# Optimization experiments

Hardware: AMD Instinct MI355X
Metric: run time of the kernel (lower is better)

Reference implementation:

```python
import jax, jax.numpy as jnp
import numpy as np

P, M, N, H, B, E, K = 50, 512, 1024, 256, 8, 400, 5
ALPHA_MAX, TAU_MAX, RHO_MAX, ETA_MAX = 0.01, 1.0, 1.0, 1.0
LEAK = 0.01  # F.leaky_relu default slope


def _lrelu(x):
    return jnp.where(x >= 0, x, LEAK * x)


def _layernorm(x, g, b, eps=1e-5):
    mu = jnp.mean(x, axis=-1, keepdims=True)
    var = jnp.mean((x - mu) ** 2, axis=-1, keepdims=True)
    return (x - mu) * jax.lax.rsqrt(var + eps) * g + b


def setup_inputs() -> dict:
    ks = iter(jax.random.split(jax.random.key(0), 16))

    def w(fin, fout):
        return jax.random.normal(next(ks), (fin, fout), jnp.float32) * np.float32(np.sqrt(2.0 / (fin + fout)))

    H4 = 4 * H
    inp = {
        'A': jax.random.normal(next(ks), (1, P, M, N), jnp.float32) * 0.05,
        'b': jax.random.normal(next(ks), (B, P, M, 1), jnp.float32),
        'W1': w(2 * N, H), 'b1': jnp.zeros(H), 'bn1_s': jnp.ones(H), 'bn1_t': jnp.zeros(H),
        'W2': w(H, 2 * H), 'b2': jnp.zeros(2 * H), 'bn2_s': jnp.ones(2 * H), 'bn2_t': jnp.zeros(2 * H),
        'W3': w(2 * H, H4), 'b3': jnp.zeros(H4), 'bn3_s': jnp.ones(H4), 'bn3_t': jnp.zeros(H4),
        'W4': w(H4, H4), 'b4': jnp.zeros(H4), 'bn4_s': jnp.ones(H4), 'bn4_t': jnp.zeros(H4),
        'W5': w(H4, H4), 'b5': jnp.zeros(H4), 'bn5_s': jnp.ones(H4), 'bn5_t': jnp.zeros(H4),
        'ln_g': jnp.ones(H4), 'ln_b': jnp.zeros(H4),
        'Wd1': w(P * H4, H4), 'bd1': jnp.zeros(H4), 'lnd1_g': jnp.ones(H4), 'lnd1_b': jnp.zeros(H4),
        'Wd2': w(H4, 2 * H), 'bd2': jnp.zeros(2 * H), 'lnd2_g': jnp.ones(2 * H), 'lnd2_b': jnp.zeros(2 * H),
        'Wd3': w(2 * H, H), 'bd3': jnp.zeros(H), 'lnd3_g': jnp.ones(H), 'lnd3_b': jnp.zeros(H),
        'Wfc': w(H, 4) * 0.1, 'bfc': jnp.zeros(4),
        'edge_index': jax.random.randint(next(ks), (2, E), 0, P),
    }
    return inp


def reference(A, b, W1, b1, bn1_s, bn1_t, W2, b2, bn2_s, bn2_t, W3, b3, bn3_s, bn3_t,
              W4, b4, bn4_s, bn4_t, W5, b5, bn5_s, bn5_t, ln_g, ln_b,
              Wd1, bd1, lnd1_g, lnd1_b, Wd2, bd2, lnd2_g, lnd2_b, Wd3, bd3, lnd3_g, lnd3_b,
              Wfc, bfc, edge_index):
    A0 = A[0]                                             # [P,M,N]
    AtA = jnp.einsum('pmi,pmj->pij', A0, A0)              # [P,N,N]  (compute_Atx(A))
    Atb = jnp.einsum('pmn,bpm->bpn', A0, b[..., 0])[..., None]  # [B,P,N,1]

    src, dst = edge_index[0], edge_index[1]
    ones_e = jnp.ones((E,), A.dtype)
    # sum_neighbors: out-degree of each node p, shape broadcastable to [B,P,1,1]
    sum_nb = jax.ops.segment_sum(ones_e, src, num_segments=P)[None, :, None, None]

    # GCNConv normalization with self loops: norm_ij = deg_i^-1/2 * deg_j^-1/2
    sl = jnp.arange(P)
    src_a = jnp.concatenate([src, sl])
    dst_a = jnp.concatenate([dst, sl])
    deg = jax.ops.segment_sum(jnp.ones((E + P,), A.dtype), dst_a, num_segments=P)
    dinv = jax.lax.rsqrt(deg)
    coef = (dinv[src_a] * dinv[dst_a])[:, None]           # [E+P,1]

    convs = [(W1, b1, bn1_s, bn1_t), (W2, b2, bn2_s, bn2_t), (W3, b3, bn3_s, bn3_t),
             (W4, b4, bn4_s, bn4_t), (W5, b5, bn5_s, bn5_t)]

    def gconv(x, W, bias):                                # x: [P,Cin]
        xw = x @ W
        return jax.ops.segment_sum(xw[src_a] * coef, dst_a, num_segments=P) + bias

    def encode_one(feat):                                 # feat: [P,2N]
        x = feat
        for (W, bias, s, t) in convs:
            # leaky_relu -> BatchNorm1d (eval: affine scale/shift) -> dropout (eval: id)
            x = _lrelu(gconv(x, W, bias)) * s + t
        return _layernorm(x, ln_g, ln_b).reshape(-1)      # [P*4H]

    enc = jax.vmap(encode_one)

    y = jnp.zeros((B, P, N, 1), A.dtype)
    U = jnp.zeros_like(y)
    delta = jnp.zeros_like(y)
    Ys = []
    for k in range(K):
        AtAy = jnp.einsum('pij,bpj->bpi', AtA, y[..., 0])[..., None]  # [B,P,N,1]
        feat = jnp.concatenate([AtAy, Atb], axis=2)[..., 0]           # [B,P,2N]
        code = enc(feat)                                              # [B,P*4H]
        h = _lrelu(_layernorm(code @ Wd1 + bd1, lnd1_g, lnd1_b))
        h = _lrelu(_layernorm(h @ Wd2 + bd2, lnd2_g, lnd2_b))
        h = _lrelu(_layernorm(h @ Wd3 + bd3, lnd3_g, lnd3_b))
        hyp = jnp.clip(jax.nn.sigmoid(h @ Wfc + bfc), 1e-4, 0.99).reshape(B, 4, 1, 1, 1)
        alpha = hyp[:, 0] * ALPHA_MAX
        tau = hyp[:, 1] * TAU_MAX
        rho = hyp[:, 2] * RHO_MAX
        eta = hyp[:, 3] * ETA_MAX
        g = AtAy - Atb + jnp.sign(y) * tau + U * sum_nb + delta * rho
        mg = max(30.0, 100.0 - k)
        g = jnp.clip(g, -mg, mg)
        mv = max(10.0, 200.0 - k * 3)
        y = jnp.clip(y - alpha * g, -mv, mv)
        # compute_delta: for each directed edge (s,d): delta[s]+= (y_s-y_d); delta[d]-= (y_s-y_d)
        diff = y[:, src] - y[:, dst]                                  # [B,E,N,1]
        delta = jnp.zeros_like(y).at[:, src].add(diff).at[:, dst].add(-diff)
        U = jnp.clip(U + delta * eta, -mv, mv)
        Ys.append(y)
    return jnp.stack(Ys)                                              # [K,B,P,N,1]
```

## Files before the change

### kernel.cpp

```cpp
#include <hip/hip_runtime.h>

#define PP 50
#define MM 512
#define NN 1024

constexpr size_t F_ATB   = 0;
constexpr size_t F_ATAY  = F_ATB   + 409600;
constexpr size_t F_Y     = F_ATAY  + 409600;
constexpr size_t F_U     = F_Y     + 409600;
constexpr size_t F_DELTA = F_U     + 409600;
constexpr size_t F_BT    = F_DELTA + 409600;
constexpr size_t F_AYT   = F_BT    + 204800;
constexpr size_t F_Z     = F_AYT   + 204800;
constexpr size_t F_X0    = F_Z     + 917504;
constexpr size_t F_X1    = F_X0    + 409600;
constexpr size_t F_CODET = F_X1    + 409600;
constexpr size_t F_PART  = F_CODET + 409600;
constexpr size_t F_DPART = F_PART  + 3670016;
constexpr size_t F_DPART2= F_DPART + 2097152;
constexpr size_t F_H1    = F_DPART2+ 32768;
constexpr size_t F_H2    = F_H1    + 8192;
constexpr size_t F_H3    = F_H2    + 4096;
constexpr size_t F_HYP   = F_H3    + 2048;
constexpr size_t F_GCCO  = F_HYP   + 64;
constexpr size_t F_SUMNB = F_GCCO  + 512;
constexpr size_t F_END   = F_SUMNB + 64;

__device__ __forceinline__ float lrelu(float v) { return v >= 0.f ? v : 0.01f * v; }

__device__ __forceinline__ void bred2(float& s1, float& s2, float* sm) {
  #pragma unroll
  for (int off = 32; off > 0; off >>= 1) {
    s1 += __shfl_down(s1, off);
    s2 += __shfl_down(s2, off);
  }
  int w = threadIdx.x >> 6, l = threadIdx.x & 63;
  if (l == 0) { sm[w] = s1; sm[4 + w] = s2; }
  __syncthreads();
  s1 = sm[0] + sm[1] + sm[2] + sm[3];
  s2 = sm[4] + sm[5] + sm[6] + sm[7];
}

__global__ __launch_bounds__(512) void ksetup(const int* __restrict__ ei, float* sumnb,
                                              float* gccoef, int* gcoff, int* gcsrc,
                                              int* nbroff, int* nbridx) {
  __shared__ int cin[PP];
  __shared__ int cou[PP];
  __shared__ float sdinv[PP];
  __shared__ int goff[PP + 1], noff[PP + 1];
  int t = threadIdx.x;
  const int* src = ei;
  const int* dst = ei + 400;
  if (t < PP) { cin[t] = 0; cou[t] = 0; }
  __syncthreads();
  if (t < 400) {
    atomicAdd(&cou[src[t]], 1);
    atomicAdd(&cin[dst[t]], 1);
  }
  __syncthreads();
  if (t < PP) {
    sdinv[t] = rsqrtf((float)(cin[t] + 1));
    sumnb[t] = (float)cou[t];
  }
  __syncthreads();
  if (t == 0) {
    goff[0] = 0; noff[0] = 0;
    for (int p = 0; p < PP; ++p) {
      goff[p + 1] = goff[p] + cin[p] + 1;
      noff[p + 1] = noff[p] + cin[p] + cou[p];
    }
  }
  __syncthreads();
  if (t <= PP) { gcoff[t] = goff[t]; nbroff[t] = noff[t]; }
  if (t < 400) {
    int d = dst[t], s = src[t];
    int slot = 0;
    for (int e = 0; e < t; ++e) slot += (dst[e] == d) ? 1 : 0;
    int pos = goff[d] + slot;
    gcsrc[pos] = s;
    gccoef[pos] = sdinv[s] * sdinv[d];
  }
  if (t < PP) {
    int pos = goff[t] + cin[t];
    gcsrc[pos] = t;
    gccoef[pos] = sdinv[t] * sdinv[t];
  }
  if (t < 400) {
    int s = src[t], d = dst[t];
    int so = 0, si = 0;
    for (int e = 0; e < t; ++e) {
      so += (src[e] == s) ? 1 : 0;
      si += (dst[e] == d) ? 1 : 0;
    }
    nbridx[noff[s] + so] = d;
    nbridx[noff[d] + cou[d] + si] = s;
  }
}

__global__ __launch_bounds__(256) void kbt(const float* __restrict__ b, float* __restrict__ bt) {
  int i = blockIdx.x * 256 + threadIdx.x;
  int bb = i / (PP * MM);
  int r = i - bb * (PP * MM);
  bt[r * 8 + bb] = b[i];
}

__global__ __launch_bounds__(256) void katz(const float* __restrict__ A, const float* __restrict__ q,
                                            float* __restrict__ outv) {
  __shared__ float red[4][64][8];
  int nb = blockIdx.x, p = blockIdx.y, t = threadIdx.x;
  int ln = t & 63, mg = t >> 6;
  int n = nb * 64 + ln;
  float acc[8] = {0, 0, 0, 0, 0, 0, 0, 0};
  const float* ap = A + ((size_t)p * MM + mg * 128) * NN + n;
  const float* qp = q + ((size_t)p * MM + mg * 128) * 8;
  for (int m0 = 0; m0 < 128; m0 += 8) {
    float av[8];
    #pragma unroll
    for (int u = 0; u < 8; ++u) av[u] = ap[(size_t)(m0 + u) * NN];
    #pragma unroll
    for (int u = 0; u < 8; ++u) {
      #pragma unroll
      for (int bb = 0; bb < 8; ++bb) acc[bb] += av[u] * qp[(m0 + u) * 8 + bb];
    }
  }
  #pragma unroll
  for (int bb = 0; bb < 8; ++bb) red[mg][ln][bb] = acc[bb];
  __syncthreads();
  if (mg == 0) {
    #pragma unroll
    for (int bb = 0; bb < 8; ++bb) {
      float v = red[0][ln][bb] + red[1][ln][bb] + red[2][ln][bb] + red[3][ln][bb];
      outv[((size_t)bb * PP + p) * NN + n] = v;
    }
  }
}

__global__ __launch_bounds__(256) void kay(const float* __restrict__ A, const float* __restrict__ y,
                                           float* __restrict__ ayt) {
  __shared__ __align__(16) float sy[8][NN];
  int p = blockIdx.x, mb = blockIdx.y, t = threadIdx.x;
  #pragma unroll
  for (int bb = 0; bb < 8; ++bb)
    for (int n = t; n < NN; n += 256) sy[bb][n] = y[(bb * PP + p) * NN + n];
  __syncthreads();
  int w = t >> 6, l = t & 63;
  int mbase = mb * 64 + w * 16;
  for (int i = 0; i < 8; ++i) {
    int m0 = mbase + 2 * i, m1 = m0 + 1;
    float acc0[8] = {0, 0, 0, 0, 0, 0, 0, 0};
    float acc1[8] = {0, 0, 0, 0, 0, 0, 0, 0};
    const float* a0p = A + ((size_t)p * MM + m0) * NN;
    const float* a1p = a0p + NN;
    #pragma unroll
    for (int jj = 0; jj < 4; ++jj) {
      int n0 = 4 * l + 256 * jj;
      float4 a0 = *(const float4*)(a0p + n0);
      float4 a1 = *(const float4*)(a1p + n0);
      #pragma unroll
      for (int bb = 0; bb < 8; ++bb) {
        float4 yv = *(const float4*)&sy[bb][n0];
        acc0[bb] += a0.x * yv.x + a0.y * yv.y + a0.z * yv.z + a0.w * yv.w;
        acc1[bb] += a1.x * yv.x + a1.y * yv.y + a1.z * yv.z + a1.w * yv.w;
      }
    }
    #pragma unroll
    for (int off = 32; off > 0; off >>= 1) {
      #pragma unroll
      for (int bb = 0; bb < 8; ++bb) {
        acc0[bb] += __shfl_down(acc0[bb], off);
        acc1[bb] += __shfl_down(acc1[bb], off);
      }
    }
    if (l == 0) {
      #pragma unroll
      for (int bb = 0; bb < 8; ++bb) {
        ayt[((size_t)p * MM + m0) * 8 + bb] = acc0[bb];
        ayt[((size_t)p * MM + m1) * 8 + bb] = acc1[bb];
      }
    }
  }
}

__global__ __launch_bounds__(256) void kgather1(const float* __restrict__ atay,
                                                const float* __restrict__ atb,
                                                float* __restrict__ z,
                                                const int* __restrict__ gcoff,
                                                const int* __restrict__ gcsrc,
                                                const float* __restrict__ gccoef, int first) {
  int r = blockIdx.x, cc = blockIdx.y, t = threadIdx.x;
  size_t zi = (size_t)r * 2048 + (size_t)cc * 256 + t;
  if (r >= 400) { z[zi] = 0.f; return; }
  int srcA = (cc < 4) ? 1 : 0;
  if (srcA && first) { z[zi] = 0.f; return; }
  int b = r / 50, p = r - b * 50;
  int c = (srcA ? cc * 256 : (cc - 4) * 256) + t;
  const float* src = srcA ? atay : atb;
  float acc = 0.f;
  int o0 = gcoff[p], o1 = gcoff[p + 1];
  for (int idx = o0; idx < o1; ++idx)
    acc += gccoef[idx] * src[((size_t)b * 50 + gcsrc[idx]) * 1024 + c];
  z[zi] = acc;
}

__global__ __launch_bounds__(256) void kgatherX(const float* __restrict__ x, float* __restrict__ z,
                                                int Cin, const int* __restrict__ gcoff,
                                                const int* __restrict__ gcsrc,
                                                const float* __restrict__ gccoef) {
  int r = blockIdx.x, cc = blockIdx.y, t = threadIdx.x;
  int c = cc * 256 + t;
  size_t zi = (size_t)r * Cin + c;
  if (r >= 400) { z[zi] = 0.f; return; }
  int b = r / 50, p = r - b * 50;
  float acc = 0.f;
  int o0 = gcoff[p], o1 = gcoff[p + 1];
  for (int idx = o0; idx < o1; ++idx)
    acc += gccoef[idx] * x[((size_t)b * 50 + gcsrc[idx]) * Cin + c];
  z[zi] = acc;
}

__global__ __launch_bounds__(256) void kgemm(const float* __restrict__ X, const float* __restrict__ W,
                                             float* __restrict__ part, int K, int C, int krange) {
  int cb = blockIdx.x, rb = blockIdx.y, s = blockIdx.z;
  int t = threadIdx.x;
  __shared__ __align__(16) float As[16][64];
  __shared__ __align__(16) float Bs[16][68];
  int rbase = rb * 64, cbase = cb * 64;
  int k0 = s * krange, kend = k0 + krange;
  float acc[4][4] = {};
  int tx = t & 15, ty = t >> 4;
  int lrow = t >> 2, lk = (t & 3) * 4;
  int brow = t >> 4, bc = (t & 15) * 4;
  for (int k = k0; k < kend; k += 16) {
    float4 av = *(const float4*)(X + (size_t)(rbase + lrow) * K + k + lk);
    As[lk + 0][lrow] = av.x;
    As[lk + 1][lrow] = av.y;
    As[lk + 2][lrow] = av.z;
    As[lk + 3][lrow] = av.w;
    *(float4*)&Bs[brow][bc] = *(const float4*)(W + (size_t)(k + brow) * C + cbase + bc);
    __syncthreads();
    #pragma unroll
    for (int kk = 0; kk < 16; ++kk) {
      float4 a = *(const float4*)&As[kk][ty * 4];
      float4 b = *(const float4*)&Bs[kk][tx * 4];
      float aa[4] = {a.x, a.y, a.z, a.w};
      float bb[4] = {b.x, b.y, b.z, b.w};
      #pragma unroll
      for (int i = 0; i < 4; ++i)
        #pragma unroll
        for (int j = 0; j < 4; ++j) acc[i][j] += aa[i] * bb[j];
    }
    __syncthreads();
  }
  #pragma unroll
  for (int i = 0; i < 4; ++i) {
    int r = rbase + ty * 4 + i;
    *(float4*)&part[((size_t)s * 448 + r) * C + cbase + tx * 4] =
        make_float4(acc[i][0], acc[i][1], acc[i][2], acc[i][3]);
  }
}

template <int NCH, bool LASTLN>
__global__ __launch_bounds__(256) void kredE(const float* __restrict__ part, int S,
                                             const float* __restrict__ bias,
                                             const float* __restrict__ bns,
                                             const float* __restrict__ bnt,
                                             float* __restrict__ xout,
                                             const float* __restrict__ lng,
                                             const float* __restrict__ lnb,
                                             float* __restrict__ codet) {
  __shared__ float smr[8];
  constexpr int C = NCH * 256;
  int r = blockIdx.x, t = threadIdx.x;
  float vals[NCH];
  #pragma unroll
  for (int ch = 0; ch < NCH; ++ch) {
    int c = ch * 256 + t;
    float acc = 0.f;
    const float* pp = part + (size_t)r * C + c;
    #pragma unroll 4
    for (int s = 0; s < S; ++s) acc += pp[(size_t)s * 448 * C];
    float v = lrelu(acc + bias[c]);
    vals[ch] = v * bns[c] + bnt[c];
  }
  if (!LASTLN) {
    #pragma unroll
    for (int ch = 0; ch < NCH; ++ch)
      xout[(size_t)r * C + ch * 256 + t] = vals[ch];
  } else {
    float s1 = 0.f, s2 = 0.f;
    #pragma unroll
    for (int ch = 0; ch < NCH; ++ch) { s1 += vals[ch]; s2 += vals[ch] * vals[ch]; }
    bred2(s1, s2, smr);
    float mu = s1 / (float)C;
    float var = s2 / (float)C - mu * mu;
    float rs = rsqrtf(var + 1e-5f);
    int b = r / 50, p = r - b * 50;
    #pragma unroll
    for (int ch = 0; ch < NCH; ++ch) {
      int c = ch * 256 + t;
      codet[((size_t)p * C + c) * 8 + b] = (vals[ch] - mu) * rs * lng[c] + lnb[c];
    }
  }
}

__global__ __launch_bounds__(256) void kwd1(const float* __restrict__ W,
                                            const float* __restrict__ in_t,
                                            float* __restrict__ dpart) {
  int t = threadIdx.x, s = blockIdx.x;
  int k0 = s * 200;
  float4 acc[8];
  #pragma unroll
  for (int b = 0; b < 8; ++b) acc[b] = make_float4(0.f, 0.f, 0.f, 0.f);
  const float* wp = W + (size_t)k0 * 1024 + 4 * t;
  const float* qp = in_t + (size_t)k0 * 8;
  for (int k = 0; k < 200; k += 4) {
    float4 wv[4], qa[4], qb[4];
    #pragma unroll
    for (int u = 0; u < 4; ++u) {
      wv[u] = *(const float4*)(wp + (size_t)(k + u) * 1024);
      qa[u] = *(const float4*)(qp + (k + u) * 8);
      qb[u] = *(const float4*)(qp + (k + u) * 8 + 4);
    }
    #pragma unroll
    for (int u = 0; u < 4; ++u) {
      float qs[8] = {qa[u].x, qa[u].y, qa[u].z, qa[u].w, qb[u].x, qb[u].y, qb[u].z, qb[u].w};
      #pragma unroll
      for (int b = 0; b < 8; ++b) {
        acc[b].x += wv[u].x * qs[b];
        acc[b].y += wv[u].y * qs[b];
        acc[b].z += wv[u].z * qs[b];
        acc[b].w += wv[u].w * qs[b];
      }
    }
  }
  #pragma unroll
  for (int b = 0; b < 8; ++b)
    *(float4*)&dpart[(size_t)(s * 8 + b) * 1024 + 4 * t] = acc[b];
}

__global__ __launch_bounds__(256) void kredA(const float* __restrict__ dpart,
                                             float* __restrict__ dpart2) {
  int cb = blockIdx.x, sg = blockIdx.y, b = blockIdx.z, t = threadIdx.x;
  int c = cb * 256 + t;
  float acc = 0.f;
  const float* pp = dpart + ((size_t)(sg * 64) * 8 + b) * 1024 + c;
  #pragma unroll 8
  for (int i = 0; i < 64; ++i) acc += pp[(size_t)i * 8 * 1024];
  dpart2[((size_t)sg * 8 + b) * 1024 + c] = acc;
}

__global__ __launch_bounds__(128) void kwdS(const float* __restrict__ W,
                                            const float* __restrict__ in_t,
                                            float* __restrict__ part, int C, int krange) {
  int t = threadIdx.x, s = blockIdx.x;
  int k0 = s * krange;
  float4 acc[8];
  #pragma unroll
  for (int b = 0; b < 8; ++b) acc[b] = make_float4(0.f, 0.f, 0.f, 0.f);
  const float* wp = W + (size_t)k0 * C + 4 * t;
  const float* qp = in_t + (size_t)k0 * 8;
  for (int k = 0; k < krange; ++k) {
    float4 wv = *(const float4*)(wp + (size_t)k * C);
    float4 qa = *(const float4*)(qp + k * 8);
    float4 qb = *(const float4*)(qp + k * 8 + 4);
    float qs[8] = {qa.x, qa.y, qa.z, qa.w, qb.x, qb.y, qb.z, qb.w};
    #pragma unroll
    for (int b = 0; b < 8; ++b) {
      acc[b].x += wv.x * qs[b];
      acc[b].y += wv.y * qs[b];
      acc[b].z += wv.z * qs[b];
      acc[b].w += wv.w * qs[b];
    }
  }
  #pragma unroll
  for (int b = 0; b < 8; ++b)
    *(float4*)&part[(size_t)(s * 8 + b) * C + 4 * t] = acc[b];
}

__global__ __launch_bounds__(1024) void kred(const float* __restrict__ part, int S, int C,
                                             const float* __restrict__ bias,
                                             const float* __restrict__ g,
                                             const float* __restrict__ be,
                                             float* __restrict__ out_t) {
  __shared__ float sm[32];
  int b = blockIdx.x, t = threadIdx.x;
  float v = bias[t];
  const float* pp = part + (size_t)b * C + t;
  #pragma unroll 4
  for (int s = 0; s < S; ++s) v += pp[(size_t)s * 8 * C];
  float s1 = v, s2 = v * v;
  #pragma unroll
  for (int off = 32; off > 0; off >>= 1) {
    s1 += __shfl_down(s1, off);
    s2 += __shfl_down(s2, off);
  }
  int w = t >> 6, l = t & 63;
  int nw = blockDim.x >> 6;
  if (l == 0) { sm[w] = s1; sm[16 + w] = s2; }
  __syncthreads();
  s1 = 0.f; s2 = 0.f;
  for (int i = 0; i < nw; ++i) { s1 += sm[i]; s2 += sm[16 + i]; }
  float inv = 1.f / (float)C;
  float mu = s1 * inv;
  float var = s2 * inv - mu * mu;
  float rs = rsqrtf(var + 1e-5f);
  float o = lrelu((v - mu) * rs * g[t] + be[t]);
  out_t[t * 8 + b] = o;
}

__global__ __launch_bounds__(256) void kwfc(const float* __restrict__ Wfc, const float* __restrict__ bfc,
                                            const float* __restrict__ h3t, float* __restrict__ hyp) {
  __shared__ float sd[32][257];
  int t = threadIdx.x;
  float4 w = *(const float4*)(Wfc + t * 4);
  #pragma unroll
  for (int bb = 0; bb < 8; ++bb) {
    float x = h3t[t * 8 + bb];
    sd[bb * 4 + 0][t] = x * w.x;
    sd[bb * 4 + 1][t] = x * w.y;
    sd[bb * 4 + 2][t] = x * w.z;
    sd[bb * 4 + 3][t] = x * w.w;
  }
  __syncthreads();
  if (t < 32) {
    float s = 0.f;
    for (int i = 0; i < 256; ++i) s += sd[t][i];
    s += bfc[t & 3];
    float sig = 1.f / (1.f + expf(-s));
    sig = fminf(fmaxf(sig, 1e-4f), 0.99f);
    hyp[t] = sig;
  }
}

__global__ __launch_bounds__(256) void kyupd(const float* __restrict__ atay, const float* __restrict__ atb,
                                             float* y, const float* __restrict__ U,
                                             const float* __restrict__ delta,
                                             const float* __restrict__ hyp,
                                             const float* __restrict__ sumnb, float* __restrict__ outp,
                                             float mg, float mv, int first) {
  int i = blockIdx.x * 256 + threadIdx.x;
  int bb = i / (PP * NN);
  int rem = i - bb * (PP * NN);
  int p = rem >> 10;
  float alpha = hyp[bb * 4 + 0] * 0.01f;
  float g;
  float yv;
  if (first) {
    yv = 0.f;
    g = -atb[i];
  } else {
    float tau = hyp[bb * 4 + 1];
    float rho = hyp[bb * 4 + 2];
    yv = y[i];
    float sg = (yv > 0.f) ? 1.f : ((yv < 0.f) ? -1.f : 0.f);
    g = atay[i] - atb[i] + sg * tau + U[i] * sumnb[p] + delta[i] * rho;
  }
  g = fminf(fmaxf(g, -mg), mg);
  float yn = yv - alpha * g;
  yn = fminf(fmaxf(yn, -mv), mv);
  y[i] = yn;
  outp[i] = yn;
}

__global__ __launch_bounds__(256) void kdeltaU(const float* __restrict__ y, float* __restrict__ delta,
                                               float* __restrict__ U, const float* __restrict__ hyp,
                                               const int* __restrict__ nbroff,
                                               const int* __restrict__ nbridx, float mv, int first) {
  int t = threadIdx.x;
  int n = blockIdx.x * 256 + t;
  int p = blockIdx.y;
  int bb = blockIdx.z;
  int o0 = nbroff[p], o1 = nbroff[p + 1];
  int base = bb * (PP * NN) + p * NN;
  float d = (float)(o1 - o0) * y[base + n];
  for (int idx = o0; idx < o1; ++idx) {
    int q = nbridx[idx];
    d -= y[bb * (PP * NN) + q * NN + n];
  }
  delta[base + n] = d;
  float eta = hyp[bb * 4 + 3];
  float u0 = first ? 0.f : U[base + n];
  float u = u0 + d * eta;
  U[base + n] = fminf(fmaxf(u, -mv), mv);
}

extern "C" void kernel_launch(void* const* d_in, const int* in_sizes, int n_in,
                              void* d_out, int out_size, void* d_ws, size_t ws_size,
                              hipStream_t stream) {
  const float* A    = (const float*)d_in[0];
  const float* bvec = (const float*)d_in[1];
  const float* W1 = (const float*)d_in[2];
  const float* b1 = (const float*)d_in[3];
  const float* bn1s = (const float*)d_in[4];
  const float* bn1t = (const float*)d_in[5];
  const float* W2 = (const float*)d_in[6];
  const float* b2 = (const float*)d_in[7];
  const float* bn2s = (const float*)d_in[8];
  const float* bn2t = (const float*)d_in[9];
  const float* W3 = (const float*)d_in[10];
  const float* b3 = (const float*)d_in[11];
  const float* bn3s = (const float*)d_in[12];
  const float* bn3t = (const float*)d_in[13];
  const float* W4 = (const float*)d_in[14];
  const float* b4 = (const float*)d_in[15];
  const float* bn4s = (const float*)d_in[16];
  const float* bn4t = (const float*)d_in[17];
  const float* W5 = (const float*)d_in[18];
  const float* b5 = (const float*)d_in[19];
  const float* bn5s = (const float*)d_in[20];
  const float* bn5t = (const float*)d_in[21];
  const float* lng = (const float*)d_in[22];
  const float* lnb = (const float*)d_in[23];
  const float* Wd1 = (const float*)d_in[24];
  const float* bd1 = (const float*)d_in[25];
  const float* lnd1g = (const float*)d_in[26];
  const float* lnd1b = (const float*)d_in[27];
  const float* Wd2 = (const float*)d_in[28];
  const float* bd2 = (const float*)d_in[29];
  const float* lnd2g = (const float*)d_in[30];
  const float* lnd2b = (const float*)d_in[31];
  const float* Wd3 = (const float*)d_in[32];
  const float* bd3 = (const float*)d_in[33];
  const float* lnd3g = (const float*)d_in[34];
  const float* lnd3b = (const float*)d_in[35];
  const float* Wfc = (const float*)d_in[36];
  const float* bfc = (const float*)d_in[37];
  const int* ei = (const int*)d_in[38];

  float* out = (float*)d_out;
  float* wsf = (float*)d_ws;
  float* atb = wsf + F_ATB;
  float* atay = wsf + F_ATAY;
  float* yb = wsf + F_Y;
  float* Ub = wsf + F_U;
  float* db = wsf + F_DELTA;
  float* bt = wsf + F_BT;
  float* ayt = wsf + F_AYT;
  float* z = wsf + F_Z;
  float* x0 = wsf + F_X0;
  float* x1 = wsf + F_X1;
  float* codet = wsf + F_CODET;
  float* part = wsf + F_PART;
  float* dpart = wsf + F_DPART;
  float* dpart2 = wsf + F_DPART2;
  float* h1t = wsf + F_H1;
  float* h2t = wsf + F_H2;
  float* h3t = wsf + F_H3;
  float* hyp = wsf + F_HYP;
  float* gccoef = wsf + F_GCCO;
  float* sumnb = wsf + F_SUMNB;
  int* wsi = (int*)(wsf + F_END);
  int* gcoff = wsi;
  int* gcsrc = wsi + 64;
  int* nbroff = wsi + 576;
  int* nbridx = wsi + 640;

  ksetup<<<1, 512, 0, stream>>>(ei, sumnb, gccoef, gcoff, gcsrc, nbroff, nbridx);
  kbt<<<800, 256, 0, stream>>>(bvec, bt);
  katz<<<dim3(16, 50), 256, 0, stream>>>(A, bt, atb);

  const float mgs[5] = {100.f, 99.f, 98.f, 97.f, 96.f};
  const float mvs[5] = {200.f, 197.f, 194.f, 191.f, 188.f};

  for (int k = 0; k < 5; ++k) {
    if (k > 0) {
      kay<<<dim3(50, 8), 256, 0, stream>>>(A, yb, ayt);
      katz<<<dim3(16, 50), 256, 0, stream>>>(A, ayt, atay);
    }
    kgather1<<<dim3(448, 8), 256, 0, stream>>>(atay, atb, z, gcoff, gcsrc, gccoef, k == 0);
    kgemm<<<dim3(4, 7, 16), 256, 0, stream>>>(z, W1, part, 2048, 256, 128);
    kredE<1, false><<<400, 256, 0, stream>>>(part, 16, b1, bn1s, bn1t, x0, nullptr, nullptr, nullptr);
    kgatherX<<<dim3(448, 1), 256, 0, stream>>>(x0, z, 256, gcoff, gcsrc, gccoef);
    kgemm<<<dim3(8, 7, 8), 256, 0, stream>>>(z, W2, part, 256, 512, 32);
    kredE<2, false><<<400, 256, 0, stream>>>(part, 8, b2, bn2s, bn2t, x1, nullptr, nullptr, nullptr);
    kgatherX<<<dim3(448, 2), 256, 0, stream>>>(x1, z, 512, gcoff, gcsrc, gccoef);
    kgemm<<<dim3(16, 7, 8), 256, 0, stream>>>(z, W3, part, 512, 1024, 64);
    kredE<4, false><<<400, 256, 0, stream>>>(part, 8, b3, bn3s, bn3t, x0, nullptr, nullptr, nullptr);
    kgatherX<<<dim3(448, 4), 256, 0, stream>>>(x0, z, 1024, gcoff, gcsrc, gccoef);
    kgemm<<<dim3(16, 7, 8), 256, 0, stream>>>(z, W4, part, 1024, 1024, 128);
    kredE<4, false><<<400, 256, 0, stream>>>(part, 8, b4, bn4s, bn4t, x1, nullptr, nullptr, nullptr);
    kgatherX<<<dim3(448, 4), 256, 0, stream>>>(x1, z, 1024, gcoff, gcsrc, gccoef);
    kgemm<<<dim3(16, 7, 8), 256, 0, stream>>>(z, W5, part, 1024, 1024, 128);
    kredE<4, true><<<400, 256, 0, stream>>>(part, 8, b5, bn5s, bn5t, nullptr, lng, lnb, codet);
    kwd1<<<256, 256, 0, stream>>>(Wd1, codet, dpart);
    kredA<<<dim3(4, 4, 8), 256, 0, stream>>>(dpart, dpart2);
    kred<<<8, 1024, 0, stream>>>(dpart2, 4, 1024, bd1, lnd1g, lnd1b, h1t);
    kwdS<<<64, 128, 0, stream>>>(Wd2, h1t, dpart, 512, 16);
    kred<<<8, 512, 0, stream>>>(dpart, 64, 512, bd2, lnd2g, lnd2b, h2t);
    kwdS<<<32, 64, 0, stream>>>(Wd3, h2t, dpart, 256, 16);
    kred<<<8, 256, 0, stream>>>(dpart, 32, 256, bd3, lnd3g, lnd3b, h3t);
    kwfc<<<1, 256, 0, stream>>>(Wfc, bfc, h3t, hyp);
    kyupd<<<1600, 256, 0, stream>>>(atay, atb, yb, Ub, db, hyp, sumnb,
                                    out + (size_t)k * 409600, mgs[k], mvs[k], k == 0);
    kdeltaU<<<dim3(4, 50, 8), 256, 0, stream>>>(yb, db, Ub, hyp, nbroff, nbridx, mvs[k], k == 0);
  }
}
```

Baseline: 1.568 ms.

## Hoist loop-invariant Atb gather, skip zero half at k=0, fuse decoder tail

The graph-conv gather of Atb does not change across iterations, so it is computed once before the loop into its own buffer, and a new GEMM kernel reads its K dimension from two separate buffers. At k=0 the Atay half is zero, so the first GEMM runs only over the Atb half. The Wd2/LN, Wd3/LN and fc/sigmoid stages are fused into one 8-block kernel, replacing five small launches. The fused tail uses only 8 blocks, so its weight streaming has little parallelism, and the dpart buffer now aliases part.

New measurement: 1.655 ms. +5.6%, slower.

```diff
diff --git a/kernel.cpp b/kernel.cpp
--- a/kernel.cpp
+++ b/kernel.cpp
@@ -11,17 +11,15 @@
 constexpr size_t F_DELTA = F_U     + 409600;
 constexpr size_t F_BT    = F_DELTA + 409600;
 constexpr size_t F_AYT   = F_BT    + 204800;
-constexpr size_t F_Z     = F_AYT   + 204800;
-constexpr size_t F_X0    = F_Z     + 917504;
+constexpr size_t F_ZA    = F_AYT   + 204800;
+constexpr size_t F_ZB    = F_ZA    + 458752;
+constexpr size_t F_X0    = F_ZB    + 458752;
 constexpr size_t F_X1    = F_X0    + 409600;
 constexpr size_t F_CODET = F_X1    + 409600;
 constexpr size_t F_PART  = F_CODET + 409600;
-constexpr size_t F_DPART = F_PART  + 3670016;
-constexpr size_t F_DPART2= F_DPART + 2097152;
+constexpr size_t F_DPART2= F_PART  + 3670016;
 constexpr size_t F_H1    = F_DPART2+ 32768;
-constexpr size_t F_H2    = F_H1    + 8192;
-constexpr size_t F_H3    = F_H2    + 4096;
-constexpr size_t F_HYP   = F_H3    + 2048;
+constexpr size_t F_HYP   = F_H1    + 8192;
 constexpr size_t F_GCCO  = F_HYP   + 64;
 constexpr size_t F_SUMNB = F_GCCO  + 512;
 constexpr size_t F_END   = F_SUMNB + 64;
@@ -179,27 +177,6 @@
       }
     }
   }
-}
-
-__global__ __launch_bounds__(256) void kgather1(const float* __restrict__ atay,
-                                                const float* __restrict__ atb,
-                                                float* __restrict__ z,
-                                                const int* __restrict__ gcoff,
-                                                const int* __restrict__ gcsrc,
-                                                const float* __restrict__ gccoef, int first) {
-  int r = blockIdx.x, cc = blockIdx.y, t = threadIdx.x;
-  size_t zi = (size_t)r * 2048 + (size_t)cc * 256 + t;
-  if (r >= 400) { z[zi] = 0.f; return; }
-  int srcA = (cc < 4) ? 1 : 0;
-  if (srcA && first) { z[zi] = 0.f; return; }
-  int b = r / 50, p = r - b * 50;
-  int c = (srcA ? cc * 256 : (cc - 4) * 256) + t;
-  const float* src = srcA ? atay : atb;
-  float acc = 0.f;
-  int o0 = gcoff[p], o1 = gcoff[p + 1];
-  for (int idx = o0; idx < o1; ++idx)
-    acc += gccoef[idx] * src[((size_t)b * 50 + gcsrc[idx]) * 1024 + c];
-  z[zi] = acc;
 }
 
 __global__ __launch_bounds__(256) void kgatherX(const float* __restrict__ x, float* __restrict__ z,
@@ -259,6 +236,51 @@
   }
 }
 
+__global__ __launch_bounds__(256) void kgemmC(const float* __restrict__ XA, const float* __restrict__ XB,
+                                              const float* __restrict__ W, float* __restrict__ part,
+                                              int C, int krange, int koff) {
+  int cb = blockIdx.x, rb = blockIdx.y, s = blockIdx.z;
+  int t = threadIdx.x;
+  __shared__ __align__(16) float As[16][64];
+  __shared__ __align__(16) float Bs[16][68];
+  int rbase = rb * 64, cbase = cb * 64;
+  int k0 = koff + s * krange, kend = k0 + krange;
+  float acc[4][4] = {};
+  int tx = t & 15, ty = t >> 4;
+  int lrow = t >> 2, lk = (t & 3) * 4;
+  int brow = t >> 4, bc = (t & 15) * 4;
+  for (int k = k0; k < kend; k += 16) {
+    int r = rbase + lrow;
+    const float* xp = (k < 1024) ? (XA + (size_t)r * 1024 + k)
+                                 : (XB + (size_t)r * 1024 + (k - 1024));
+    float4 av = *(const float4*)(xp + lk);
+    As[lk + 0][lrow] = av.x;
+    As[lk + 1][lrow] = av.y;
+    As[lk + 2][lrow] = av.z;
+    As[lk + 3][lrow] = av.w;
+    *(float4*)&Bs[brow][bc] = *(const float4*)(W + (size_t)(k + brow) * C + cbase + bc);
+    __syncthreads();
+    #pragma unroll
+    for (int kk = 0; kk < 16; ++kk) {
+      float4 a = *(const float4*)&As[kk][ty * 4];
+      float4 b = *(const float4*)&Bs[kk][tx * 4];
+      float aa[4] = {a.x, a.y, a.z, a.w};
+      float bb[4] = {b.x, b.y, b.z, b.w};
+      #pragma unroll
+      for (int i = 0; i < 4; ++i)
+        #pragma unroll
+        for (int j = 0; j < 4; ++j) acc[i][j] += aa[i] * bb[j];
+    }
+    __syncthreads();
+  }
+  #pragma unroll
+  for (int i = 0; i < 4; ++i) {
+    int r = rbase + ty * 4 + i;
+    *(float4*)&part[((size_t)s * 448 + r) * C + cbase + tx * 4] =
+        make_float4(acc[i][0], acc[i][1], acc[i][2], acc[i][3]);
+  }
+}
+
 template <int NCH, bool LASTLN>
 __global__ __launch_bounds__(256) void kredE(const float* __restrict__ part, int S,
                                              const float* __restrict__ bias,
@@ -349,34 +371,6 @@
   dpart2[((size_t)sg * 8 + b) * 1024 + c] = acc;
 }
 
-__global__ __launch_bounds__(128) void kwdS(const float* __restrict__ W,
-                                            const float* __restrict__ in_t,
-                                            float* __restrict__ part, int C, int krange) {
-  int t = threadIdx.x, s = blockIdx.x;
-  int k0 = s * krange;
-  float4 acc[8];
-  #pragma unroll
-  for (int b = 0; b < 8; ++b) acc[b] = make_float4(0.f, 0.f, 0.f, 0.f);
-  const float* wp = W + (size_t)k0 * C + 4 * t;
-  const float* qp = in_t + (size_t)k0 * 8;
-  for (int k = 0; k < krange; ++k) {
-    float4 wv = *(const float4*)(wp + (size_t)k * C);
-    float4 qa = *(const float4*)(qp + k * 8);
-    float4 qb = *(const float4*)(qp + k * 8 + 4);
-    float qs[8] = {qa.x, qa.y, qa.z, qa.w, qb.x, qb.y, qb.z, qb.w};
-    #pragma unroll
-    for (int b = 0; b < 8; ++b) {
-      acc[b].x += wv.x * qs[b];
-      acc[b].y += wv.y * qs[b];
-      acc[b].z += wv.z * qs[b];
-      acc[b].w += wv.w * qs[b];
-    }
-  }
-  #pragma unroll
-  for (int b = 0; b < 8; ++b)
-    *(float4*)&part[(size_t)(s * 8 + b) * C + 4 * t] = acc[b];
-}
-
 __global__ __launch_bounds__(1024) void kred(const float* __restrict__ part, int S, int C,
                                              const float* __restrict__ bias,
                                              const float* __restrict__ g,
@@ -408,27 +402,87 @@
   out_t[t * 8 + b] = o;
 }
 
-__global__ __launch_bounds__(256) void kwfc(const float* __restrict__ Wfc, const float* __restrict__ bfc,
-                                            const float* __restrict__ h3t, float* __restrict__ hyp) {
-  __shared__ float sd[32][257];
-  int t = threadIdx.x;
-  float4 w = *(const float4*)(Wfc + t * 4);
-  #pragma unroll
-  for (int bb = 0; bb < 8; ++bb) {
-    float x = h3t[t * 8 + bb];
-    sd[bb * 4 + 0][t] = x * w.x;
-    sd[bb * 4 + 1][t] = x * w.y;
-    sd[bb * 4 + 2][t] = x * w.z;
-    sd[bb * 4 + 3][t] = x * w.w;
-  }
-  __syncthreads();
-  if (t < 32) {
-    float s = 0.f;
-    for (int i = 0; i < 256; ++i) s += sd[t][i];
-    s += bfc[t & 3];
+__global__ __launch_bounds__(256) void kdtail(const float* __restrict__ Wd2,
+                                              const float* __restrict__ bd2,
+                                              const float* __restrict__ g2,
+                                              const float* __restrict__ be2,
+                                              const float* __restrict__ Wd3,
+                                              const float* __restrict__ bd3,
+                                              const float* __restrict__ g3,
+                                              const float* __restrict__ be3,
+                                              const float* __restrict__ Wfc,
+                                              const float* __restrict__ bfc,
+                                              const float* __restrict__ h1t,
+                                              float* __restrict__ hyp) {
+  __shared__ float sh1[1024];
+  __shared__ float sh2[512];
+  __shared__ float sh3[256];
+  __shared__ float smr[8];
+  __shared__ float sfc[16];
+  int b = blockIdx.x, t = threadIdx.x;
+  for (int i = t; i < 1024; i += 256) sh1[i] = h1t[i * 8 + b];
+  __syncthreads();
+  float a0 = bd2[t], a1 = bd2[t + 256];
+  for (int k = 0; k < 1024; k += 4) {
+    const float* wp = Wd2 + (size_t)k * 512 + t;
+    float x0 = sh1[k], x1 = sh1[k + 1], x2 = sh1[k + 2], x3 = sh1[k + 3];
+    float w00 = wp[0],    w01 = wp[256];
+    float w10 = wp[512],  w11 = wp[768];
+    float w20 = wp[1024], w21 = wp[1280];
+    float w30 = wp[1536], w31 = wp[1792];
+    a0 += x0 * w00; a1 += x0 * w01;
+    a0 += x1 * w10; a1 += x1 * w11;
+    a0 += x2 * w20; a1 += x2 * w21;
+    a0 += x3 * w30; a1 += x3 * w31;
+  }
+  {
+    float s1 = a0 + a1, s2 = a0 * a0 + a1 * a1;
+    bred2(s1, s2, smr);
+    float mu = s1 * (1.f / 512.f);
+    float var = s2 * (1.f / 512.f) - mu * mu;
+    float rs = rsqrtf(var + 1e-5f);
+    sh2[t] = lrelu((a0 - mu) * rs * g2[t] + be2[t]);
+    sh2[t + 256] = lrelu((a1 - mu) * rs * g2[t + 256] + be2[t + 256]);
+  }
+  __syncthreads();
+  float a = bd3[t];
+  for (int k = 0; k < 512; k += 4) {
+    const float* wp = Wd3 + (size_t)k * 256 + t;
+    a += sh2[k] * wp[0];
+    a += sh2[k + 1] * wp[256];
+    a += sh2[k + 2] * wp[512];
+    a += sh2[k + 3] * wp[768];
+  }
+  {
+    float s1 = a, s2 = a * a;
+    bred2(s1, s2, smr);
+    float mu = s1 * (1.f / 256.f);
+    float var = s2 * (1.f / 256.f) - mu * mu;
+    float rs = rsqrtf(var + 1e-5f);
+    sh3[t] = lrelu((a - mu) * rs * g3[t] + be3[t]);
+  }
+  __syncthreads();
+  float4 wv = *(const float4*)(Wfc + t * 4);
+  float x = sh3[t];
+  float p0 = x * wv.x, p1 = x * wv.y, p2 = x * wv.z, p3 = x * wv.w;
+  #pragma unroll
+  for (int off = 32; off > 0; off >>= 1) {
+    p0 += __shfl_down(p0, off);
+    p1 += __shfl_down(p1, off);
+    p2 += __shfl_down(p2, off);
+    p3 += __shfl_down(p3, off);
+  }
+  int w = t >> 6, l = t & 63;
+  if (l == 0) {
+    sfc[w * 4 + 0] = p0; sfc[w * 4 + 1] = p1;
+    sfc[w * 4 + 2] = p2; sfc[w * 4 + 3] = p3;
+  }
+  __syncthreads();
+  if (t < 4) {
+    float s = sfc[t] + sfc[4 + t] + sfc[8 + t] + sfc[12 + t] + bfc[t];
     float sig = 1.f / (1.f + expf(-s));
     sig = fminf(fmaxf(sig, 1e-4f), 0.99f);
-    hyp[t] = sig;
+    hyp[b * 4 + t] = sig;
   }
 }
 
@@ -443,8 +497,7 @@
   int rem = i - bb * (PP * NN);
   int p = rem >> 10;
   float alpha = hyp[bb * 4 + 0] * 0.01f;
-  float g;
-  float yv;
+  float g, yv;
   if (first) {
     yv = 0.f;
     g = -atb[i];
@@ -536,16 +589,15 @@
   float* db = wsf + F_DELTA;
   float* bt = wsf + F_BT;
   float* ayt = wsf + F_AYT;
-  float* z = wsf + F_Z;
+  float* zA = wsf + F_ZA;
+  float* zB = wsf + F_ZB;
   float* x0 = wsf + F_X0;
   float* x1 = wsf + F_X1;
   float* codet = wsf + F_CODET;
   float* part = wsf + F_PART;
-  float* dpart = wsf + F_DPART;
+  float* dpart = part;
   float* dpart2 = wsf + F_DPART2;
   float* h1t = wsf + F_H1;
-  float* h2t = wsf + F_H2;
-  float* h3t = wsf + F_H3;
   float* hyp = wsf + F_HYP;
   float* gccoef = wsf + F_GCCO;
   float* sumnb = wsf + F_SUMNB;
@@ -558,6 +610,7 @@
   ksetup<<<1, 512, 0, stream>>>(ei, sumnb, gccoef, gcoff, gcsrc, nbroff, nbridx);
   kbt<<<800, 256, 0, stream>>>(bvec, bt);
   katz<<<dim3(16, 50), 256, 0, stream>>>(A, bt, atb);
+  kgatherX<<<dim3(448, 4), 256, 0, stream>>>(atb, zB, 1024, gcoff, gcsrc, gccoef);
 
   const float mgs[5] = {100.f, 99.f, 98.f, 97.f, 96.f};
   const float mvs[5] = {200.f, 197.f, 194.f, 191.f, 188.f};
@@ -567,29 +620,31 @@
       kay<<<dim3(50, 8), 256, 0, stream>>>(A, yb, ayt);
       katz<<<dim3(16, 50), 256, 0, stream>>>(A, ayt, atay);
     }
-    kgather1<<<dim3(448, 8), 256, 0, stream>>>(atay, atb, z, gcoff, gcsrc, gccoef, k == 0);
-    kgemm<<<dim3(4, 7, 16), 256, 0, stream>>>(z, W1, part, 2048, 256, 128);
-    kredE<1, false><<<400, 256, 0, stream>>>(part, 16, b1, bn1s, bn1t, x0, nullptr, nullptr, nullptr);
-    kgatherX<<<dim3(448, 1), 256, 0, stream>>>(x0, z, 256, gcoff, gcsrc, gccoef);
-    kgemm<<<dim3(8, 7, 8), 256, 0, stream>>>(z, W2, part, 256, 512, 32);
+    if (k == 0) {
+      kgemmC<<<dim3(4, 7, 8), 256, 0, stream>>>(zA, zB, W1, part, 256, 128, 1024);
+      kredE<1, false><<<400, 256, 0, stream>>>(part, 8, b1, bn1s, bn1t, x0, nullptr, nullptr, nullptr);
+    } else {
+      kgatherX<<<dim3(448, 4), 256, 0, stream>>>(atay, zA, 1024, gcoff, gcsrc, gccoef);
+      kgemmC<<<dim3(4, 7, 16), 256, 0, stream>>>(zA, zB, W1, part, 256, 128, 0);
+      kredE<1, false><<<400, 256, 0, stream>>>(part, 16, b1, bn1s, bn1t, x0, nullptr, nullptr, nullptr);
+    }
+    kgatherX<<<dim3(448, 1), 256, 0, stream>>>(x0, zA, 256, gcoff, gcsrc, gccoef);
+    kgemm<<<dim3(8, 7, 8), 256, 0, stream>>>(zA, W2, part, 256, 512, 32);
     kredE<2, false><<<400, 256, 0, stream>>>(part, 8, b2, bn2s, bn2t, x1, nullptr, nullptr, nullptr);
-    kgatherX<<<dim3(448, 2), 256, 0, stream>>>(x1, z, 512, gcoff, gcsrc, gccoef);
-    kgemm<<<dim3(16, 7, 8), 256, 0, stream>>>(z, W3, part, 512, 1024, 64);
+    kgatherX<<<dim3(448, 2), 256, 0, stream>>>(x1, zA, 512, gcoff, gcsrc, gccoef);
+    kgemm<<<dim3(16, 7, 8), 256, 0, stream>>>(zA, W3, part, 512, 1024, 64);
     kredE<4, false><<<400, 256, 0, stream>>>(part, 8, b3, bn3s, bn3t, x0, nullptr, nullptr, nullptr);
-    kgatherX<<<dim3(448, 4), 256, 0, stream>>>(x0, z, 1024, gcoff, gcsrc, gccoef);
-    kgemm<<<dim3(16, 7, 8), 256, 0, stream>>>(z, W4, part, 1024, 1024, 128);
+    kgatherX<<<dim3(448, 4), 256, 0, stream>>>(x0, zA, 1024, gcoff, gcsrc, gccoef);
+    kgemm<<<dim3(16, 7, 8), 256, 0, stream>>>(zA, W4, part, 1024, 1024, 128);
     kredE<4, false><<<400, 256, 0, stream>>>(part, 8, b4, bn4s, bn4t, x1, nullptr, nullptr, nullptr);
-    kgatherX<<<dim3(448, 4), 256, 0, stream>>>(x1, z, 1024, gcoff, gcsrc, gccoef);
-    kgemm<<<dim3(16, 7, 8), 256, 0, stream>>>(z, W5, part, 1024, 1024, 128);
+    kgatherX<<<dim3(448, 4), 256, 0, stream>>>(x1, zA, 1024, gcoff, gcsrc, gccoef);
+    kgemm<<<dim3(16, 7, 8), 256, 0, stream>>>(zA, W5, part, 1024, 1024, 128);
     kredE<4, true><<<400, 256, 0, stream>>>(part, 8, b5, bn5s, bn5t, nullptr, lng, lnb, codet);
     kwd1<<<256, 256, 0, stream>>>(Wd1, codet, dpart);
     kredA<<<dim3(4, 4, 8), 256, 0, stream>>>(dpart, dpart2);
     kred<<<8, 1024, 0, stream>>>(dpart2, 4, 1024, bd1, lnd1g, lnd1b, h1t);
-    kwdS<<<64, 128, 0, stream>>>(Wd2, h1t, dpart, 512, 16);
-    kred<<<8, 512, 0, stream>>>(dpart, 64, 512, bd2, lnd2g, lnd2b, h2t);
-    kwdS<<<32, 64, 0, stream>>>(Wd3, h2t, dpart, 256, 16);
-    kred<<<8, 256, 0, stream>>>(dpart, 32, 256, bd3, lnd3g, lnd3b, h3t);
-    kwfc<<<1, 256, 0, stream>>>(Wfc, bfc, h3t, hyp);
+    kdtail<<<8, 256, 0, stream>>>(Wd2, bd2, lnd2g, lnd2b, Wd3, bd3, lnd3g, lnd3b,
+                                  Wfc, bfc, h1t, hyp);
     kyupd<<<1600, 256, 0, stream>>>(atay, atb, yb, Ub, db, hyp, sumnb,
                                     out + (size_t)k * 409600, mgs[k], mvs[k], k == 0);
     kdeltaU<<<dim3(4, 50, 8), 256, 0, stream>>>(yb, db, Ub, hyp, nbroff, nbridx, mvs[k], k == 0);
```

## Hoist loop-invariant Atb gather and skip zero half of first encoder GEMM

Applied to the files above, without the earlier changes.

The graph-conv gather of Atb, which does not change across iterations, now runs once before the loop into its own buffer. A new two-source GEMM reads the Atay and Atb halves directly. On the first iteration Atay is zero, so that GEMM covers only the Atb half of K. The split-K factors of the encoder GEMMs are also halved (8→4), which means fewer partial sums to write and reduce but less parallelism per launch; the dpart buffer now aliases part to save workspace.

After: 1.591 ms. About the same (+1.4%).

```diff
diff --git a/kernel.cpp b/kernel.cpp
--- a/kernel.cpp
+++ b/kernel.cpp
@@ -11,13 +11,13 @@
 constexpr size_t F_DELTA = F_U     + 409600;
 constexpr size_t F_BT    = F_DELTA + 409600;
 constexpr size_t F_AYT   = F_BT    + 204800;
-constexpr size_t F_Z     = F_AYT   + 204800;
-constexpr size_t F_X0    = F_Z     + 917504;
+constexpr size_t F_ZA    = F_AYT   + 204800;
+constexpr size_t F_ZB    = F_ZA    + 458752;
+constexpr size_t F_X0    = F_ZB    + 458752;
 constexpr size_t F_X1    = F_X0    + 409600;
 constexpr size_t F_CODET = F_X1    + 409600;
 constexpr size_t F_PART  = F_CODET + 409600;
-constexpr size_t F_DPART = F_PART  + 3670016;
-constexpr size_t F_DPART2= F_DPART + 2097152;
+constexpr size_t F_DPART2= F_PART  + 3670016;
 constexpr size_t F_H1    = F_DPART2+ 32768;
 constexpr size_t F_H2    = F_H1    + 8192;
 constexpr size_t F_H3    = F_H2    + 4096;
@@ -179,27 +179,6 @@
       }
     }
   }
-}
-
-__global__ __launch_bounds__(256) void kgather1(const float* __restrict__ atay,
-                                                const float* __restrict__ atb,
-                                                float* __restrict__ z,
-                                                const int* __restrict__ gcoff,
-                                                const int* __restrict__ gcsrc,
-                                                const float* __restrict__ gccoef, int first) {
-  int r = blockIdx.x, cc = blockIdx.y, t = threadIdx.x;
-  size_t zi = (size_t)r * 2048 + (size_t)cc * 256 + t;
-  if (r >= 400) { z[zi] = 0.f; return; }
-  int srcA = (cc < 4) ? 1 : 0;
-  if (srcA && first) { z[zi] = 0.f; return; }
-  int b = r / 50, p = r - b * 50;
-  int c = (srcA ? cc * 256 : (cc - 4) * 256) + t;
-  const float* src = srcA ? atay : atb;
-  float acc = 0.f;
-  int o0 = gcoff[p], o1 = gcoff[p + 1];
-  for (int idx = o0; idx < o1; ++idx)
-    acc += gccoef[idx] * src[((size_t)b * 50 + gcsrc[idx]) * 1024 + c];
-  z[zi] = acc;
 }
 
 __global__ __launch_bounds__(256) void kgatherX(const float* __restrict__ x, float* __restrict__ z,
@@ -259,6 +238,51 @@
   }
 }
 
+__global__ __launch_bounds__(256) void kgemmC(const float* __restrict__ XA, const float* __restrict__ XB,
+                                              const float* __restrict__ W, float* __restrict__ part,
+                                              int C, int krange, int koff) {
+  int cb = blockIdx.x, rb = blockIdx.y, s = blockIdx.z;
+  int t = threadIdx.x;
+  __shared__ __align__(16) float As[16][64];
+  __shared__ __align__(16) float Bs[16][68];
+  int rbase = rb * 64, cbase = cb * 64;
+  int k0 = koff + s * krange, kend = k0 + krange;
+  float acc[4][4] = {};
+  int tx = t & 15, ty = t >> 4;
+  int lrow = t >> 2, lk = (t & 3) * 4;
+  int brow = t >> 4, bc = (t & 15) * 4;
+  for (int k = k0; k < kend; k += 16) {
+    int r = rbase + lrow;
+    const float* xp = (k < 1024) ? (XA + (size_t)r * 1024 + k)
+                                 : (XB + (size_t)r * 1024 + (k - 1024));
+    float4 av = *(const float4*)(xp + lk);
+    As[lk + 0][lrow] = av.x;
+    As[lk + 1][lrow] = av.y;
+    As[lk + 2][lrow] = av.z;
+    As[lk + 3][lrow] = av.w;
+    *(float4*)&Bs[brow][bc] = *(const float4*)(W + (size_t)(k + brow) * C + cbase + bc);
+    __syncthreads();
+    #pragma unroll
+    for (int kk = 0; kk < 16; ++kk) {
+      float4 a = *(const float4*)&As[kk][ty * 4];
+      float4 b = *(const float4*)&Bs[kk][tx * 4];
+      float aa[4] = {a.x, a.y, a.z, a.w};
+      float bb[4] = {b.x, b.y, b.z, b.w};
+      #pragma unroll
+      for (int i = 0; i < 4; ++i)
+        #pragma unroll
+        for (int j = 0; j < 4; ++j) acc[i][j] += aa[i] * bb[j];
+    }
+    __syncthreads();
+  }
+  #pragma unroll
+  for (int i = 0; i < 4; ++i) {
+    int r = rbase + ty * 4 + i;
+    *(float4*)&part[((size_t)s * 448 + r) * C + cbase + tx * 4] =
+        make_float4(acc[i][0], acc[i][1], acc[i][2], acc[i][3]);
+  }
+}
+
 template <int NCH, bool LASTLN>
 __global__ __launch_bounds__(256) void kredE(const float* __restrict__ part, int S,
                                              const float* __restrict__ bias,
@@ -443,8 +467,7 @@
   int rem = i - bb * (PP * NN);
   int p = rem >> 10;
   float alpha = hyp[bb * 4 + 0] * 0.01f;
-  float g;
-  float yv;
+  float g, yv;
   if (first) {
     yv = 0.f;
     g = -atb[i];
@@ -536,12 +559,13 @@
   float* db = wsf + F_DELTA;
   float* bt = wsf + F_BT;
   float* ayt = wsf + F_AYT;
-  float* z = wsf + F_Z;
+  float* zA = wsf + F_ZA;
+  float* zB = wsf + F_ZB;
   float* x0 = wsf + F_X0;
   float* x1 = wsf + F_X1;
   float* codet = wsf + F_CODET;
   float* part = wsf + F_PART;
-  float* dpart = wsf + F_DPART;
+  float* dpart = part;
   float* dpart2 = wsf + F_DPART2;
   float* h1t = wsf + F_H1;
   float* h2t = wsf + F_H2;
@@ -558,6 +582,7 @@
   ksetup<<<1, 512, 0, stream>>>(ei, sumnb, gccoef, gcoff, gcsrc, nbroff, nbridx);
   kbt<<<800, 256, 0, stream>>>(bvec, bt);
   katz<<<dim3(16, 50), 256, 0, stream>>>(A, bt, atb);
+  kgatherX<<<dim3(448, 4), 256, 0, stream>>>(atb, zB, 1024, gcoff, gcsrc, gccoef);
 
   const float mgs[5] = {100.f, 99.f, 98.f, 97.f, 96.f};
   const float mvs[5] = {200.f, 197.f, 194.f, 191.f, 188.f};
@@ -567,21 +592,26 @@
       kay<<<dim3(50, 8), 256, 0, stream>>>(A, yb, ayt);
       katz<<<dim3(16, 50), 256, 0, stream>>>(A, ayt, atay);
     }
-    kgather1<<<dim3(448, 8), 256, 0, stream>>>(atay, atb, z, gcoff, gcsrc, gccoef, k == 0);
-    kgemm<<<dim3(4, 7, 16), 256, 0, stream>>>(z, W1, part, 2048, 256, 128);
-    kredE<1, false><<<400, 256, 0, stream>>>(part, 16, b1, bn1s, bn1t, x0, nullptr, nullptr, nullptr);
-    kgatherX<<<dim3(448, 1), 256, 0, stream>>>(x0, z, 256, gcoff, gcsrc, gccoef);
-    kgemm<<<dim3(8, 7, 8), 256, 0, stream>>>(z, W2, part, 256, 512, 32);
-    kredE<2, false><<<400, 256, 0, stream>>>(part, 8, b2, bn2s, bn2t, x1, nullptr, nullptr, nullptr);
-    kgatherX<<<dim3(448, 2), 256, 0, stream>>>(x1, z, 512, gcoff, gcsrc, gccoef);
-    kgemm<<<dim3(16, 7, 8), 256, 0, stream>>>(z, W3, part, 512, 1024, 64);
-    kredE<4, false><<<400, 256, 0, stream>>>(part, 8, b3, bn3s, bn3t, x0, nullptr, nullptr, nullptr);
-    kgatherX<<<dim3(448, 4), 256, 0, stream>>>(x0, z, 1024, gcoff, gcsrc, gccoef);
-    kgemm<<<dim3(16, 7, 8), 256, 0, stream>>>(z, W4, part, 1024, 1024, 128);
-    kredE<4, false><<<400, 256, 0, stream>>>(part, 8, b4, bn4s, bn4t, x1, nullptr, nullptr, nullptr);
-    kgatherX<<<dim3(448, 4), 256, 0, stream>>>(x1, z, 1024, gcoff, gcsrc, gccoef);
-    kgemm<<<dim3(16, 7, 8), 256, 0, stream>>>(z, W5, part, 1024, 1024, 128);
-    kredE<4, true><<<400, 256, 0, stream>>>(part, 8, b5, bn5s, bn5t, nullptr, lng, lnb, codet);
+    if (k == 0) {
+      kgemmC<<<dim3(4, 7, 4), 256, 0, stream>>>(zA, zB, W1, part, 256, 256, 1024);
+      kredE<1, false><<<400, 256, 0, stream>>>(part, 4, b1, bn1s, bn1t, x0, nullptr, nullptr, nullptr);
+    } else {
+      kgatherX<<<dim3(448, 4), 256, 0, stream>>>(atay, zA, 1024, gcoff, gcsrc, gccoef);
+      kgemmC<<<dim3(4, 7, 8), 256, 0, stream>>>(zA, zB, W1, part, 256, 256, 0);
+      kredE<1, false><<<400, 256, 0, stream>>>(part, 8, b1, bn1s, bn1t, x0, nullptr, nullptr, nullptr);
+    }
+    kgatherX<<<dim3(448, 1), 256, 0, stream>>>(x0, zA, 256, gcoff, gcsrc, gccoef);
+    kgemm<<<dim3(8, 7, 4), 256, 0, stream>>>(zA, W2, part, 256, 512, 64);
+    kredE<2, false><<<400, 256, 0, stream>>>(part, 4, b2, bn2s, bn2t, x1, nullptr, nullptr, nullptr);
+    kgatherX<<<dim3(448, 2), 256, 0, stream>>>(x1, zA, 512, gcoff, gcsrc, gccoef);
+    kgemm<<<dim3(16, 7, 4), 256, 0, stream>>>(zA, W3, part, 512, 1024, 128);
+    kredE<4, false><<<400, 256, 0, stream>>>(part, 4, b3, bn3s, bn3t, x0, nullptr, nullptr, nullptr);
+    kgatherX<<<dim3(448, 4), 256, 0, stream>>>(x0, zA, 1024, gcoff, gcsrc, gccoef);
+    kgemm<<<dim3(16, 7, 4), 256, 0, stream>>>(zA, W4, part, 1024, 1024, 256);
+    kredE<4, false><<<400, 256, 0, stream>>>(part, 4, b4, bn4s, bn4t, x1, nullptr, nullptr, nullptr);
+    kgatherX<<<dim3(448, 4), 256, 0, stream>>>(x1, zA, 1024, gcoff, gcsrc, gccoef);
+    kgemm<<<dim3(16, 7, 4), 256, 0, stream>>>(zA, W5, part, 1024, 1024, 256);
+    kredE<4, true><<<400, 256, 0, stream>>>(part, 4, b5, bn5s, bn5t, nullptr, lng, lnb, codet);
     kwd1<<<256, 256, 0, stream>>>(Wd1, codet, dpart);
     kredA<<<dim3(4, 4, 8), 256, 0, stream>>>(dpart, dpart2);
     kred<<<8, 1024, 0, stream>>>(dpart2, 4, 1024, bd1, lnd1g, lnd1b, h1t);
```
